# Performance work log

Measured on AMD Instinct MI355X. Metric: run time of the kernel, lower is better.

## Reference

```python
import jax, jax.numpy as jnp
import numpy as np
from math import factorial as fact

# openmx, nao_max=14: row = col = 1x0e+1x0e+1x0e+1x1o+1x1o+1x2e (dim 14)
NAO = 14
LS = [0, 0, 0, 1, 1, 2]
IDX_CHANGE = np.array([0, 1, 2, 5, 3, 4, 8, 6, 7, 11, 13, 9, 12, 10])
IDX_INV = np.empty(NAO, dtype=np.int64)
IDX_INV[IDX_CHANGE] = np.arange(NAO)


def _su2_cg(j1, m1, j2, m2, j3, m3):
    # SU(2) Clebsch-Gordan coefficient <j1 m1 j2 m2 | j3 m3> (Racah formula, e3nn convention)
    if m3 != m1 + m2:
        return 0.0
    vmin = max(-j1 + j2 + m3, -j1 + m1, 0)
    vmax = min(j2 + j3 + m1, j3 - j1 + j2, j3 + m3)
    c = ((2 * j3 + 1) * fact(j3 + j1 - j2) * fact(j3 - j1 + j2) * fact(j1 + j2 - j3)
         * fact(j3 + m3) * fact(j3 - m3)
         / (fact(j1 + j2 + j3 + 1) * fact(j1 - m1) * fact(j1 + m1)
            * fact(j2 - m2) * fact(j2 + m2))) ** 0.5
    s = 0.0
    for v in range(vmin, vmax + 1):
        s += (-1) ** (v + j2 + m2) * fact(j2 + j3 + m1 - v) * fact(j1 - m1 + v) / (
            fact(v) * fact(j3 - j1 + j2 - v) * fact(j3 + m3 - v) * fact(v + j1 - j2 - m3))
    return c * s


def _q_real_to_complex(l):
    # change of basis real spherical harmonics -> complex (e3nn convention, incl. (-i)^l phase)
    q = np.zeros((2 * l + 1, 2 * l + 1), dtype=np.complex128)
    for m in range(-l, 0):
        q[l + m, l + abs(m)] = 1 / 2 ** 0.5
        q[l + m, l - abs(m)] = -1j / 2 ** 0.5
    q[l, l] = 1
    for m in range(1, l + 1):
        q[l + m, l + abs(m)] = (-1) ** m / 2 ** 0.5
        q[l + m, l - abs(m)] = 1j * (-1) ** m / 2 ** 0.5
    return (-1j) ** l * q


def wigner_3j(l1, l2, l3):
    # real-basis Wigner 3j tensor (norm 1), shape (2l1+1, 2l2+1, 2l3+1)
    csu2 = np.zeros((2 * l1 + 1, 2 * l2 + 1, 2 * l3 + 1))
    for m1 in range(-l1, l1 + 1):
        for m2 in range(-l2, l2 + 1):
            m3 = m1 + m2
            if -l3 <= m3 <= l3:
                csu2[l1 + m1, l2 + m2, l3 + m3] = _su2_cg(l1, m1, l2, m2, l3, m3)
    q1, q2, q3 = _q_real_to_complex(l1), _q_real_to_complex(l2), _q_real_to_complex(l3)
    cc = np.einsum('ia,kb,nc,ikn->abc', q1, q2, np.conj(q3), csu2)
    c = cc.real if np.linalg.norm(cc.real) >= np.linalg.norm(cc.imag) else cc.imag
    return c / np.linalg.norm(c)


def _build_blocks():
    # enumerate all (li, lj, L) blocks in source order and compute sorted-irreps permutation
    blocks = []   # (row_start, n_rows, col_start, n_cols, cg[2L+1, 2li+1, 2lj+1])
    irreps = []   # (L, parity) of each output block
    rs = 0
    for li in LS:
        nr = 2 * li + 1
        cs = 0
        for lj in LS:
            nc = 2 * lj + 1
            for L in range(abs(li - lj), li + lj + 1):
                blocks.append((rs, nr, cs, nc, wigner_3j(L, li, lj)))
                irreps.append((L, (-1) ** (li + lj)))
            cs += nc
        rs += nr
    # e3nn Irreps.sort: stable sort by (l, parity); inv[k] = original index of k-th sorted block
    inv_perm = sorted(range(len(irreps)), key=lambda i: irreps[i])
    return blocks, inv_perm

BLOCKS, INV_PERM = _build_blocks()


def setup_inputs() -> dict:
    key = jax.random.key(0)
    x = jax.random.normal(key, (500000, NAO, NAO), dtype=jnp.float32)
    return {"x": x}


def reference(x):
    x = x.reshape(-1, NAO, NAO)
    # _change_index_inv: openmx has no minus_index (double negation cancels), only inverse permute
    x = x[:, IDX_INV[:, None], IDX_INV[None, :]]
    outs = []
    for rs, nr, cs, nc, cg in BLOCKS:
        blk = x[:, rs:rs + nr, cs:cs + nc]              # [N, 2li+1, 2lj+1]
        outs.append(jnp.einsum('nij,kij->nk', blk, jnp.asarray(cg, x.dtype)))
    return jnp.concatenate([outs[i] for i in INV_PERM], axis=-1)  # [N, 196]
```

## Files before the change

kernel.cpp:

```cpp
#include <hip/hip_runtime.h>
#include <utility>

#define NAO   14
#define NOUT  196
#define NBLK  56
#define TS    64
#define ROWP  197
#define OSTR  29
#define MAXW  28


struct Meta { int L, li, lj, rs, cs, off; };
constexpr Meta META[NBLK] = {
  {0,0,0,0,0,0},{0,0,0,0,1,1},{0,0,0,0,2,2},{1,0,1,0,3,14},{1,0,1,0,6,17},{2,0,2,0,9,97},
  {0,0,0,1,0,3},{0,0,0,1,1,4},{0,0,0,1,2,5},{1,0,1,1,3,20},{1,0,1,1,6,23},{2,0,2,1,9,102},
  {0,0,0,2,0,6},{0,0,0,2,1,7},{0,0,0,2,2,8},{1,0,1,2,3,26},{1,0,1,2,6,29},{2,0,2,2,9,107},
  {1,1,0,3,0,32},{1,1,0,3,1,35},{1,1,0,3,2,38},
  {0,1,1,3,3,9},{1,1,1,3,3,62},{2,1,1,3,3,112},
  {0,1,1,3,6,10},{1,1,1,3,6,65},{2,1,1,3,6,117},
  {1,1,2,3,9,41},{2,1,2,3,9,77},{3,1,2,3,9,152},
  {1,1,0,6,0,44},{1,1,0,6,1,47},{1,1,0,6,2,50},
  {0,1,1,6,3,11},{1,1,1,6,3,68},{2,1,1,6,3,122},
  {0,1,1,6,6,12},{1,1,1,6,6,71},{2,1,1,6,6,127},
  {1,1,2,6,9,53},{2,1,2,6,9,82},{3,1,2,6,9,159},
  {2,2,0,9,0,132},{2,2,0,9,1,137},{2,2,0,9,2,142},
  {1,2,1,9,3,56},{2,2,1,9,3,87},{3,2,1,9,3,166},
  {1,2,1,9,6,59},{2,2,1,9,6,92},{3,2,1,9,6,173},
  {0,2,2,9,9,13},{1,2,2,9,9,74},{2,2,2,9,9,147},{3,2,2,9,9,180},{4,2,2,9,9,187}
};
constexpr int IDXINV[NAO] = {0,1,2,4,5,3,7,8,6,11,13,9,12,10};

constexpr double cfact(int n){ double r=1.0; for (int i=2;i<=n;++i) r*=(double)i; return r; }
constexpr double csqrt(double x){
  if (x<=0.0) return 0.0;
  double g = x>1.0 ? x : 1.0;
  for (int i=0;i<200;++i){ double ng = 0.5*(g + x/g); if (ng==g) break; g=ng; }
  return g;
}

constexpr double su2_cg(int j1,int m1,int j2,int m2,int j3,int m3){
  if (m3 != m1+m2) return 0.0;
  int vmin = -j1+j2+m3; if (-j1+m1>vmin) vmin=-j1+m1; if (0>vmin) vmin=0;
  int vmax = j2+j3+m1;  if (j3-j1+j2<vmax) vmax=j3-j1+j2; if (j3+m3<vmax) vmax=j3+m3;
  if (vmax < vmin) return 0.0;
  double c = csqrt((2.0*j3+1.0)*cfact(j3+j1-j2)*cfact(j3-j1+j2)*cfact(j1+j2-j3)*
                   cfact(j3+m3)*cfact(j3-m3) /
                   (cfact(j1+j2+j3+1)*cfact(j1-m1)*cfact(j1+m1)*cfact(j2-m2)*cfact(j2+m2)));
  double s = 0.0;
  for (int v=vmin; v<=vmax; ++v){
    double t = cfact(j2+j3+m1-v)*cfact(j1-m1+v) /
               (cfact(v)*cfact(j3-j1+j2-v)*cfact(j3+m3-v)*cfact(v+j1-j2-m3));
    s += (((v+j2+m2)&1) ? -1.0 : 1.0) * t;
  }
  return c*s;
}

struct QMat { double re[81]; double im[81]; };
constexpr QMat build_q(int l){
  QMat q{};
  int n = 2*l+1;
  const double is2 = 0.70710678118654752440;
  for (int m=-l; m<0; ++m){ q.re[(l+m)*n+(l-m)] = is2; q.im[(l+m)*n+(l+m)] = -is2; }
  q.re[l*n+l] = 1.0;
  for (int m=1; m<=l; ++m){
    double sgn = (m&1) ? -1.0 : 1.0;
    q.re[(l+m)*n+(l+m)] = sgn*is2;
    q.im[(l+m)*n+(l-m)] = sgn*is2;
  }
  int ph = l & 3;
  if (ph){
    for (int t=0; t<n*n; ++t){
      double a=q.re[t], b=q.im[t];
      if (ph==1)      { q.re[t]= b; q.im[t]=-a; }
      else if (ph==2) { q.re[t]=-a; q.im[t]=-b; }
      else            { q.re[t]=-b; q.im[t]= a; }
    }
  }
  return q;
}

struct BlockCG { double v[225]; };
constexpr BlockCG build_block_cg(int L,int li,int lj){
  int n1=2*L+1, n2=2*li+1, n3=2*lj+1;
  double csu2[225] = {};
  for (int i=0;i<n1;++i)
    for (int k=0;k<n2;++k){
      int m1=i-L, m2=k-li, m3=m1+m2;
      if (m3>=-lj && m3<=lj)
        csu2[(i*n2+k)*n3 + (m3+lj)] = su2_cg(L,m1,li,m2,lj,m3);
    }
  QMat q1 = build_q(L), q2 = build_q(li), q3 = build_q(lj);
  double ccr[225] = {}, cci[225] = {};
  double re2=0.0, im2=0.0;
  for (int a=0;a<n1;++a)
    for (int b=0;b<n2;++b)
      for (int c=0;c<n3;++c){
        double accr=0.0, acci=0.0;
        for (int i=0;i<n1;++i){
          double ar=q1.re[i*n1+a], ai=q1.im[i*n1+a];
          if (ar==0.0 && ai==0.0) continue;
          for (int k=0;k<n2;++k){
            double br=q2.re[k*n2+b], bi=q2.im[k*n2+b];
            if (br==0.0 && bi==0.0) continue;
            double pr=ar*br-ai*bi, pi=ar*bi+ai*br;
            for (int n=0;n<n3;++n){
              double w = csu2[(i*n2+k)*n3+n];
              if (w==0.0) continue;
              double cr = q3.re[n*n3+c], ci = -q3.im[n*n3+c];
              accr += w*(pr*cr - pi*ci);
              acci += w*(pr*ci + pi*cr);
            }
          }
        }
        ccr[(a*n2+b)*n3+c]=accr; cci[(a*n2+b)*n3+c]=acci;
        re2 += accr*accr; im2 += acci*acci;
      }
  BlockCG out{};
  bool pick_re = csqrt(re2) >= csqrt(im2);
  double inv = 1.0 / csqrt(pick_re ? re2 : im2);
  for (int t=0; t<n1*n2*n3; ++t) out.v[t] = (pick_re ? ccr[t] : cci[t]) * inv;
  return out;
}

template<int B> struct BlockV {
  static constexpr BlockCG cg = build_block_cg(META[B].L, META[B].li, META[B].lj);
};

struct Tables {
  int   nnz[NOUT];
  int   cols[NOUT][MAXW];
  float wts[NOUT][MAXW];
  bool  ok;
};

template<int... Bs>
constexpr Tables build_tables_impl(std::integer_sequence<int,Bs...>){
  const BlockCG cgs[NBLK] = { BlockV<Bs>::cg... };
  Tables t{};
  bool seen[NOUT] = {};
  t.ok = true;
  for (int b=0; b<NBLK; ++b){
    int n1=2*META[b].L+1, n2=2*META[b].li+1, n3=2*META[b].lj+1;
    for (int k=0; k<n1; ++k){
      int p = META[b].off + k;
      if (p < 0 || p >= NOUT || seen[p]) { t.ok = false; continue; }
      seen[p] = true;
      int q = 0;
      for (int i=0;i<n2;++i)
        for (int j=0;j<n3;++j){
          double v = cgs[b].v[(k*n2+i)*n3+j];
          if (v > 1e-10 || v < -1e-10){
            if (q >= MAXW) { t.ok = false; continue; }
            int col = IDXINV[META[b].rs+i]*NAO + IDXINV[META[b].cs+j];
            if (col < 0 || col >= NOUT) t.ok = false;
            t.cols[p][q] = col;
            t.wts[p][q]  = (float)v;
            ++q;
          }
        }
      t.nnz[p] = q;
    }
  }
  for (int p=0;p<NOUT;++p) if (!seen[p] || t.nnz[p] < 1) t.ok = false;
  return t;
}
constexpr Tables TBL = build_tables_impl(std::make_integer_sequence<int,NBLK>{});
static_assert(TBL.ok, "Wigner CSR table build failed consistency checks");


template<int P>
__device__ __forceinline__ float dot_row(const float* __restrict__ row){
  float acc = 0.f;
  #pragma unroll
  for (int q = 0; q < TBL.nnz[P]; ++q)
    acc = fmaf(TBL.wts[P][q], row[TBL.cols[P][q]], acc);
  return acc;
}

template<int P0, int... PC>
__device__ __forceinline__ void compute_pack(const float* __restrict__ row,
                                             float* __restrict__ obl,
                                             std::integer_sequence<int,PC...>){
  ((obl[PC] = dot_row<P0+PC>(row)), ...);
}

template<int CH>
__device__ __forceinline__ void store_chunk(const float* __restrict__ ob,
                                            float* __restrict__ out,
                                            int base, int p0, int lane, int total){
  constexpr int Q = CH/4;
  #pragma unroll
  for (int it=0; it<Q; ++it){
    int t  = lane + 64*it;
    int s  = t / Q;
    int i4 = t - Q*s;
    int gf = base + s*NOUT + p0 + 4*i4;
    if (gf < total){
      const float* o = ob + s*OSTR + 4*i4;
      float4 v; v.x=o[0]; v.y=o[1]; v.z=o[2]; v.w=o[3];
      *(float4*)&out[gf] = v;
    }
  }
}

template<int W>
__device__ __forceinline__ void wave_work(const float* __restrict__ row,
                                          float* __restrict__ obw,
                                          int lane, float* __restrict__ out,
                                          int base, int total){
  constexpr int P0 = 48*W;
  constexpr int C2 = (W==3) ? 28 : 24;
  compute_pack<P0>(row, obw + lane*OSTR, std::make_integer_sequence<int,24>{});
  store_chunk<24>(obw, out, base, P0, lane, total);
  compute_pack<P0+24>(row, obw + lane*OSTR, std::make_integer_sequence<int,C2>{});
  store_chunk<C2>(obw, out, base, P0+24, lane, total);
}

__global__ __launch_bounds__(256, 2)
void expand_kernel(const float* __restrict__ x, float* __restrict__ out, int total){
  __shared__ float xs[TS*ROWP];
  __shared__ float obuf[4][64*OSTR];

  const int tid  = threadIdx.x;
  const int lane = tid & 63;
  const int wid  = tid >> 6;
  const int base = blockIdx.x * (TS*NOUT);

  for (int t4 = tid; t4 < TS*49; t4 += 256){
    int g = base + 4*t4;
    float4 v = make_float4(0.f,0.f,0.f,0.f);
    if (g < total) v = ((const float4*)x)[(base>>2) + t4];
    int s  = t4/49, i4 = t4 - 49*s;
    int w0 = s*ROWP + 4*i4;
    xs[w0] = v.x; xs[w0+1] = v.y; xs[w0+2] = v.z; xs[w0+3] = v.w;
  }
  __syncthreads();

  const float* row = &xs[lane*ROWP];
  float* ob = obuf[wid];
  switch (wid){
    case 0: wave_work<0>(row, ob, lane, out, base, total); break;
    case 1: wave_work<1>(row, ob, lane, out, base, total); break;
    case 2: wave_work<2>(row, ob, lane, out, base, total); break;
    default: wave_work<3>(row, ob, lane, out, base, total); break;
  }
}

extern "C" void kernel_launch(void* const* d_in, const int* in_sizes, int n_in,
                              void* d_out, int out_size, void* d_ws, size_t ws_size,
                              hipStream_t stream) {
  const float* x = (const float*)d_in[0];
  float* out = (float*)d_out;
  int total   = in_sizes[0];
  int nsamp   = total / NOUT;
  int nblocks = (nsamp + TS - 1) / TS;
  expand_kernel<<<dim3(nblocks), dim3(256), 0, stream>>>(x, out, total);
}
```

Before: 685.8 us.

## Use 8 waves with register accumulators and in-place swizzled LDS output staging

Doubles the block to 512 threads (8 waves) with unevenly split output ranges per wave so the nonzero work is balanced. Each wave keeps its outputs in registers, then after a barrier writes them back into the input LDS tile, which is reused as the output staging buffer. The separate per-wave output buffer is removed. A permutation of float4 slots (3a mod 49) is applied to the LDS layout to reduce bank conflicts in the staging and per-lane row reads. This trades extra barriers and up to 56 live accumulators per thread for higher occupancy and less shared memory.

Result: faster. 618.8 us (-9.8%).

```diff
diff --git a/kernel.cpp b/kernel.cpp
--- a/kernel.cpp
+++ b/kernel.cpp
@@ -6,8 +6,8 @@
 #define NBLK  56
 #define TS    64
 #define ROWP  197
-#define OSTR  29
 #define MAXW  28
+#define NTHR  512
 
 
 struct Meta { int L, li, lj, rs, cs, off; };
@@ -126,6 +126,9 @@
   static constexpr BlockCG cg = build_block_cg(META[B].L, META[B].li, META[B].lj);
 };
 
+constexpr int tau_map(int a){ return (3*a) % 49; }
+constexpr int sig_map(int c){ return 4*tau_map(c>>2) + (c&3); }
+
 struct Tables {
   int   nnz[NOUT];
   int   cols[NOUT][MAXW];
@@ -153,7 +156,7 @@
             if (q >= MAXW) { t.ok = false; continue; }
             int col = IDXINV[META[b].rs+i]*NAO + IDXINV[META[b].cs+j];
             if (col < 0 || col >= NOUT) t.ok = false;
-            t.cols[p][q] = col;
+            t.cols[p][q] = sig_map(col);
             t.wts[p][q]  = (float)v;
             ++q;
           }
@@ -167,9 +170,12 @@
 constexpr Tables TBL = build_tables_impl(std::make_integer_sequence<int,NBLK>{});
 static_assert(TBL.ok, "Wigner CSR table build failed consistency checks");
 
+constexpr int NWAVE = 8;
+constexpr int WBEG[NWAVE+1] = {0,56,77,94,128,154,171,185,196};
+
 
 template<int P>
-__device__ __forceinline__ float dot_row(const float* __restrict__ row){
+__device__ __forceinline__ float dot_row(const float* row){
   float acc = 0.f;
   #pragma unroll
   for (int q = 0; q < TBL.nnz[P]; ++q)
@@ -177,72 +183,87 @@
   return acc;
 }
 
-template<int P0, int... PC>
-__device__ __forceinline__ void compute_pack(const float* __restrict__ row,
-                                             float* __restrict__ obl,
-                                             std::integer_sequence<int,PC...>){
-  ((obl[PC] = dot_row<P0+PC>(row)), ...);
-}
-
-template<int CH>
-__device__ __forceinline__ void store_chunk(const float* __restrict__ ob,
-                                            float* __restrict__ out,
-                                            int base, int p0, int lane, int total){
-  constexpr int Q = CH/4;
-  #pragma unroll
-  for (int it=0; it<Q; ++it){
-    int t  = lane + 64*it;
-    int s  = t / Q;
-    int i4 = t - Q*s;
-    int gf = base + s*NOUT + p0 + 4*i4;
-    if (gf < total){
-      const float* o = ob + s*OSTR + 4*i4;
-      float4 v; v.x=o[0]; v.y=o[1]; v.z=o[2]; v.w=o[3];
-      *(float4*)&out[gf] = v;
-    }
-  }
-}
-
+template<int W, int... I>
+__device__ __forceinline__ void wave_compute_impl(const float* row, float* acc,
+                                                  std::integer_sequence<int,I...>){
+  ((acc[I] = dot_row<WBEG[W]+I>(row)), ...);
+}
 template<int W>
-__device__ __forceinline__ void wave_work(const float* __restrict__ row,
-                                          float* __restrict__ obw,
-                                          int lane, float* __restrict__ out,
-                                          int base, int total){
-  constexpr int P0 = 48*W;
-  constexpr int C2 = (W==3) ? 28 : 24;
-  compute_pack<P0>(row, obw + lane*OSTR, std::make_integer_sequence<int,24>{});
-  store_chunk<24>(obw, out, base, P0, lane, total);
-  compute_pack<P0+24>(row, obw + lane*OSTR, std::make_integer_sequence<int,C2>{});
-  store_chunk<C2>(obw, out, base, P0+24, lane, total);
-}
-
-__global__ __launch_bounds__(256, 2)
+__device__ __forceinline__ void wave_compute(const float* row, float* acc){
+  wave_compute_impl<W>(row, acc,
+      std::make_integer_sequence<int, WBEG[W+1]-WBEG[W]>{});
+}
+
+template<int W, int... I>
+__device__ __forceinline__ void wave_store_impl(float* xrow, const float* acc,
+                                                std::integer_sequence<int,I...>){
+  ((xrow[sig_map(WBEG[W]+I)] = acc[I]), ...);
+}
+template<int W>
+__device__ __forceinline__ void wave_store(float* xrow, const float* acc){
+  wave_store_impl<W>(xrow, acc,
+      std::make_integer_sequence<int, WBEG[W+1]-WBEG[W]>{});
+}
+
+__device__ __forceinline__ int tau_rt(int a){
+  int t3 = 3*a;
+  t3 -= (t3 >= 98) ? 98 : ((t3 >= 49) ? 49 : 0);
+  return t3;
+}
+
+__global__ __launch_bounds__(NTHR, 4)
 void expand_kernel(const float* __restrict__ x, float* __restrict__ out, int total){
   __shared__ float xs[TS*ROWP];
-  __shared__ float obuf[4][64*OSTR];
 
   const int tid  = threadIdx.x;
   const int lane = tid & 63;
   const int wid  = tid >> 6;
   const int base = blockIdx.x * (TS*NOUT);
 
-  for (int t4 = tid; t4 < TS*49; t4 += 256){
+  for (int t4 = tid; t4 < TS*49; t4 += NTHR){
     int g = base + 4*t4;
     float4 v = make_float4(0.f,0.f,0.f,0.f);
     if (g < total) v = ((const float4*)x)[(base>>2) + t4];
-    int s  = t4/49, i4 = t4 - 49*s;
-    int w0 = s*ROWP + 4*i4;
-    xs[w0] = v.x; xs[w0+1] = v.y; xs[w0+2] = v.z; xs[w0+3] = v.w;
+    int s = t4/49, a = t4 - 49*s;
+    float* w = &xs[s*ROWP + 4*tau_rt(a)];
+    w[0]=v.x; w[1]=v.y; w[2]=v.z; w[3]=v.w;
   }
   __syncthreads();
 
   const float* row = &xs[lane*ROWP];
-  float* ob = obuf[wid];
+  float acc[56];
   switch (wid){
-    case 0: wave_work<0>(row, ob, lane, out, base, total); break;
-    case 1: wave_work<1>(row, ob, lane, out, base, total); break;
-    case 2: wave_work<2>(row, ob, lane, out, base, total); break;
-    default: wave_work<3>(row, ob, lane, out, base, total); break;
+    case 0: wave_compute<0>(row, acc); break;
+    case 1: wave_compute<1>(row, acc); break;
+    case 2: wave_compute<2>(row, acc); break;
+    case 3: wave_compute<3>(row, acc); break;
+    case 4: wave_compute<4>(row, acc); break;
+    case 5: wave_compute<5>(row, acc); break;
+    case 6: wave_compute<6>(row, acc); break;
+    default: wave_compute<7>(row, acc); break;
+  }
+  __syncthreads();
+
+  float* xrow = &xs[lane*ROWP];
+  switch (wid){
+    case 0: wave_store<0>(xrow, acc); break;
+    case 1: wave_store<1>(xrow, acc); break;
+    case 2: wave_store<2>(xrow, acc); break;
+    case 3: wave_store<3>(xrow, acc); break;
+    case 4: wave_store<4>(xrow, acc); break;
+    case 5: wave_store<5>(xrow, acc); break;
+    case 6: wave_store<6>(xrow, acc); break;
+    default: wave_store<7>(xrow, acc); break;
+  }
+  __syncthreads();
+
+  for (int t4 = tid; t4 < TS*49; t4 += NTHR){
+    int gf = base + 4*t4;
+    if (gf >= total) break;
+    int s = t4/49, a = t4 - 49*s;
+    const float* o = &xs[s*ROWP + 4*tau_rt(a)];
+    float4 v; v.x=o[0]; v.y=o[1]; v.z=o[2]; v.w=o[3];
+    *(float4*)&out[gf] = v;
   }
 }
 
@@ -254,5 +275,5 @@
   int total   = in_sizes[0];
   int nsamp   = total / NOUT;
   int nblocks = (nsamp + TS - 1) / TS;
-  expand_kernel<<<dim3(nblocks), dim3(256), 0, stream>>>(x, out, total);
-}
+  expand_kernel<<<dim3(nblocks), dim3(NTHR), 0, stream>>>(x, out, total);
+}
```
